# Kernel tuning notes

Measured on AMD Instinct MI355X. Metric: run time of the kernel, lower is better.

Reference implementation:

```python
import jax, jax.numpy as jnp
import numpy as np


def setup_inputs() -> dict:
    key = jax.random.key(0)
    k1, k2, k3 = jax.random.split(key, 3)
    vol_shape = (4, 1, 128, 192, 192)   # [B, C, D, H, W]
    dsc_shape = (4, 1, 8, 12, 12)       # PatchGAN-style discriminator logits
    return {
        "dsc_fake": jax.random.normal(k1, dsc_shape, dtype=jnp.float32),
        "predicts": jax.random.normal(k2, vol_shape, dtype=jnp.float32),
        "y_data": jax.random.normal(k3, vol_shape, dtype=jnp.float32),
        "zeros": jnp.zeros(dsc_shape, dtype=jnp.float32),
    }


def reference(dsc_fake, predicts, y_data, zeros):
    # BCE with logits (stable form), target = zeros
    bce = jnp.mean(
        jnp.maximum(dsc_fake, 0.0) - dsc_fake * zeros
        + jnp.log1p(jnp.exp(-jnp.abs(dsc_fake)))
    )
    # L1 loss between target volume and prediction
    g_loss_l1 = jnp.mean(jnp.abs(y_data - predicts))
    # Finite-difference gradient MSE along D, H, W (axes 2,3,4).
    # Original detaches to numpy, so this term carries no gradient.
    yd = jax.lax.stop_gradient(y_data)
    pr = jax.lax.stop_gradient(predicts)
    g_loss_gd = jnp.float32(0.0)
    for ax in (2, 3, 4):
        gy = jnp.abs(jnp.gradient(yd, axis=ax))   # central diff interior, one-sided edges
        gp = jnp.abs(jnp.gradient(pr, axis=ax))
        g_loss_gd = g_loss_gd + jnp.mean((gy - gp) ** 2)
    return bce + 100.0 * g_loss_l1 + 100.0 * g_loss_gd
```

## Files before the change

kernel.cpp:

```cpp
#include <hip/hip_runtime.h>
#include <math.h>

namespace {
constexpr int BATCH = 4;
constexpr int DDIM  = 128;
constexpr int HDIM  = 192;
constexpr int WDIM  = 192;
constexpr long long NTOT = (long long)BATCH * DDIM * HDIM * WDIM;
constexpr int GW   = WDIM / 4;
constexpr int HS4  = GW;
constexpr int DS4  = GW * HDIM;
constexpr int NDSC = 4 * 1 * 8 * 12 * 12;
constexpr int BLOCK = 256;
constexpr int DC    = 8;
constexpr int NCH   = DDIM / DC;
constexpr int NCOL  = BATCH * HDIM * GW;
constexpr int NTHREADS = NCOL * NCH;
constexpr int GRID  = NTHREADS / BLOCK;
}

__device__ __forceinline__ float4 ld4(const float* __restrict__ p, long long g) {
    return *(const float4*)(p + 4LL * g);
}

__global__ __launch_bounds__(BLOCK) void vol_kernel(const float* __restrict__ p,
                                                    const float* __restrict__ y,
                                                    float* __restrict__ part) {
    const int t    = blockIdx.x * BLOCK + threadIdx.x;
    const int lane = threadIdx.x & 63;
    const int gw   = t % GW;
    int rest       = t / GW;
    const int h    = rest % HDIM; rest /= HDIM;
    const int b    = rest % BATCH;
    const int d0   = (rest / BATCH) * DC;

    const int   hmo = (h > 0)        ? HS4 : 0;
    const int   hpo = (h < HDIM - 1) ? HS4 : 0;
    const float sh  = (h == 0 || h == HDIM - 1) ? 1.f : 0.5f;
    const float swx = (gw == 0)      ? 1.f : 0.5f;
    const float sww = (gw == GW - 1) ? 1.f : 0.5f;
    const bool needL = (lane == 0)  && (gw > 0);
    const bool needR = (lane == 63) && (gw < GW - 1);

    long long g = (((long long)b * DDIM + d0) * HDIM + h) * GW + gw;

    const long long gm = g - ((d0 > 0) ? DS4 : 0);
    float4 ym = ld4(y, gm), pm = ld4(p, gm);
    float4 yc = ld4(y, g),  pc = ld4(p, g);
    long long gn = g + DS4;
    float4 yn = ld4(y, gn), pn = ld4(p, gn);
    float4 yhm = ld4(y, g - hmo), yhp = ld4(y, g + hpo);
    float4 phm = ld4(p, g - hmo), php = ld4(p, g + hpo);
    float eLy = 0.f, eLp = 0.f, eRy = 0.f, eRp = 0.f;
    if (needL) { eLy = y[4LL * g - 1]; eLp = p[4LL * g - 1]; }
    if (needR) { eRy = y[4LL * g + 4]; eRp = p[4LL * g + 4]; }

    float l1 = 0.f, gd = 0.f;

    #pragma unroll
    for (int i = 0; i < DC; ++i) {
        const int d = d0 + i;

        float4 ynn, pnn, yhm2, yhp2, phm2, php2;
        float eLy2 = 0.f, eLp2 = 0.f, eRy2 = 0.f, eRp2 = 0.f;
        long long gnn = gn;
        if (i < DC - 1) {
            gnn = gn + ((d + 2 < DDIM) ? DS4 : 0);
            ynn  = ld4(y, gnn);      pnn  = ld4(p, gnn);
            yhm2 = ld4(y, gn - hmo); yhp2 = ld4(y, gn + hpo);
            phm2 = ld4(p, gn - hmo); php2 = ld4(p, gn + hpo);
            if (needL) { eLy2 = y[4LL * gn - 1]; eLp2 = p[4LL * gn - 1]; }
            if (needR) { eRy2 = y[4LL * gn + 4]; eRp2 = p[4LL * gn + 4]; }
        }

        const float sd = (d == 0 || d == DDIM - 1) ? 1.f : 0.5f;

        float Ly = __shfl_up(yc.w, 1, 64);
        float Lp = __shfl_up(pc.w, 1, 64);
        float Ry = __shfl_down(yc.x, 1, 64);
        float Rp = __shfl_down(pc.x, 1, 64);
        Ly = (lane == 0)  ? eLy : Ly;   Ly = gw ? Ly : yc.x;
        Lp = (lane == 0)  ? eLp : Lp;   Lp = gw ? Lp : pc.x;
        Ry = (lane == 63) ? eRy : Ry;   Ry = (gw == GW - 1) ? yc.w : Ry;
        Rp = (lane == 63) ? eRp : Rp;   Rp = (gw == GW - 1) ? pc.w : Rp;

        l1 += fabsf(yc.x - pc.x) + fabsf(yc.y - pc.y)
            + fabsf(yc.z - pc.z) + fabsf(yc.w - pc.w);

        float t0, gy, gp;
        gy = (yc.y - Ly) * swx;   gp = (pc.y - Lp) * swx;
        t0 = fabsf(gy) - fabsf(gp); gd += t0 * t0;
        gy = (yc.z - yc.x) * 0.5f; gp = (pc.z - pc.x) * 0.5f;
        t0 = fabsf(gy) - fabsf(gp); gd += t0 * t0;
        gy = (yc.w - yc.y) * 0.5f; gp = (pc.w - pc.y) * 0.5f;
        t0 = fabsf(gy) - fabsf(gp); gd += t0 * t0;
        gy = (Ry - yc.z) * sww;   gp = (Rp - pc.z) * sww;
        t0 = fabsf(gy) - fabsf(gp); gd += t0 * t0;

        t0 = fabsf((yhp.x - yhm.x) * sh) - fabsf((php.x - phm.x) * sh); gd += t0 * t0;
        t0 = fabsf((yhp.y - yhm.y) * sh) - fabsf((php.y - phm.y) * sh); gd += t0 * t0;
        t0 = fabsf((yhp.z - yhm.z) * sh) - fabsf((php.z - phm.z) * sh); gd += t0 * t0;
        t0 = fabsf((yhp.w - yhm.w) * sh) - fabsf((php.w - phm.w) * sh); gd += t0 * t0;

        t0 = fabsf((yn.x - ym.x) * sd) - fabsf((pn.x - pm.x) * sd); gd += t0 * t0;
        t0 = fabsf((yn.y - ym.y) * sd) - fabsf((pn.y - pm.y) * sd); gd += t0 * t0;
        t0 = fabsf((yn.z - ym.z) * sd) - fabsf((pn.z - pm.z) * sd); gd += t0 * t0;
        t0 = fabsf((yn.w - ym.w) * sd) - fabsf((pn.w - pm.w) * sd); gd += t0 * t0;

        if (i < DC - 1) {
            ym = yc; yc = yn; yn = ynn;
            pm = pc; pc = pn; pn = pnn;
            yhm = yhm2; yhp = yhp2; phm = phm2; php = php2;
            eLy = eLy2; eLp = eLp2; eRy = eRy2; eRp = eRp2;
            g = gn; gn = gnn;
        }
    }

    __shared__ float lds1[4], lds2[4];
    #pragma unroll
    for (int off = 32; off > 0; off >>= 1) {
        l1 += __shfl_down(l1, off, 64);
        gd += __shfl_down(gd, off, 64);
    }
    if ((threadIdx.x & 63) == 0) {
        lds1[threadIdx.x >> 6] = l1;
        lds2[threadIdx.x >> 6] = gd;
    }
    __syncthreads();
    if (threadIdx.x == 0) {
        part[2 * blockIdx.x]     = lds1[0] + lds1[1] + lds1[2] + lds1[3];
        part[2 * blockIdx.x + 1] = lds2[0] + lds2[1] + lds2[2] + lds2[3];
    }
}

__global__ __launch_bounds__(BLOCK) void finalize_kernel(const float* __restrict__ dsc,
                                                         const float* __restrict__ part,
                                                         float* __restrict__ out) {
    float l1 = 0.f, gd = 0.f, s = 0.f;
    for (int i = threadIdx.x; i < GRID; i += BLOCK) {
        l1 += part[2 * i];
        gd += part[2 * i + 1];
    }
    for (int i = threadIdx.x; i < NDSC; i += BLOCK) {
        const float x = dsc[i];
        s += fmaxf(x, 0.f) + log1pf(expf(-fabsf(x)));
    }
    __shared__ float a[4], c[4], e[4];
    #pragma unroll
    for (int off = 32; off > 0; off >>= 1) {
        l1 += __shfl_down(l1, off, 64);
        gd += __shfl_down(gd, off, 64);
        s  += __shfl_down(s,  off, 64);
    }
    if ((threadIdx.x & 63) == 0) {
        const int w = threadIdx.x >> 6;
        a[w] = l1; c[w] = gd; e[w] = s;
    }
    __syncthreads();
    if (threadIdx.x == 0) {
        const float bce = (e[0] + e[1] + e[2] + e[3]) / (float)NDSC;
        const float l1m = (a[0] + a[1] + a[2] + a[3]) / (float)NTOT;
        const float gdm = (c[0] + c[1] + c[2] + c[3]) / (float)NTOT;
        out[0] = bce + 100.f * (l1m + gdm);
    }
}

extern "C" void kernel_launch(void* const* d_in, const int* in_sizes, int n_in,
                              void* d_out, int out_size, void* d_ws, size_t ws_size,
                              hipStream_t stream) {
    const float* dsc_fake = (const float*)d_in[0];
    const float* predicts = (const float*)d_in[1];
    const float* y_data   = (const float*)d_in[2];
    float* part = (float*)d_ws;
    float* out  = (float*)d_out;

    vol_kernel<<<GRID, BLOCK, 0, stream>>>(predicts, y_data, part);
    finalize_kernel<<<1, BLOCK, 0, stream>>>(dsc_fake, part, out);
}
```

Measured before the change: 195.2 us.

## Stage H-tile planes in LDS with async global_load_lds triple buffering

Each block now owns an 8-row H tile (plus halo rows) across a 16-deep D chunk. It stages every D plane of y and p into LDS with global_load_lds, rotating three buffers so the plane two steps ahead loads while the current one is computed. H-neighbour, D-neighbour and W edge values are read from LDS instead of repeated global loads, which removes the redundant neighbour traffic of the per-thread streaming version. In exchange it adds a block barrier per D step, reloads halo rows, and runs 384-thread blocks with a large LDS footprint that may limit occupancy.

```diff
diff --git a/kernel.cpp b/kernel.cpp
--- a/kernel.cpp
+++ b/kernel.cpp
@@ -7,94 +7,127 @@
 constexpr int HDIM  = 192;
 constexpr int WDIM  = 192;
 constexpr long long NTOT = (long long)BATCH * DDIM * HDIM * WDIM;
-constexpr int GW   = WDIM / 4;
-constexpr int HS4  = GW;
-constexpr int DS4  = GW * HDIM;
-constexpr int NDSC = 4 * 1 * 8 * 12 * 12;
-constexpr int BLOCK = 256;
-constexpr int DC    = 8;
-constexpr int NCH   = DDIM / DC;
-constexpr int NCOL  = BATCH * HDIM * GW;
-constexpr int NTHREADS = NCOL * NCH;
-constexpr int GRID  = NTHREADS / BLOCK;
+constexpr int GW    = WDIM / 4;
+constexpr int NDSC  = 4 * 1 * 8 * 12 * 12;
+constexpr int TH    = 8;
+constexpr int SROWS = TH + 2;
+constexpr int SGRP  = SROWS * GW;
+constexpr int SFL   = SGRP * 4;
+constexpr int BLOCK = TH * GW;
+constexpr int NWAVE = BLOCK / 64;
+constexpr int NCHUNK = (SGRP + 63) / 64;
+constexpr int DC    = 16;
+constexpr int GRID  = BATCH * (HDIM / TH) * (DDIM / DC);
 }
 
 __device__ __forceinline__ float4 ld4(const float* __restrict__ p, long long g) {
     return *(const float4*)(p + 4LL * g);
+}
+
+__device__ __forceinline__ void stage(const float* __restrict__ vol, long long fbase,
+                                      float* lds, int wave, int lane) {
+    for (int c = wave; c < NCHUNK; c += NWAVE) {
+        const int gbase = (c == NCHUNK - 1) ? (SGRP - 64) : (c * 64);
+        const float* g = vol + fbase + 4LL * (gbase + lane);
+        __builtin_amdgcn_global_load_lds(
+            (const __attribute__((address_space(1))) void*)g,
+            (__attribute__((address_space(3))) void*)(lds + 4 * gbase),
+            16, 0, 0);
+    }
 }
 
 __global__ __launch_bounds__(BLOCK) void vol_kernel(const float* __restrict__ p,
                                                     const float* __restrict__ y,
                                                     float* __restrict__ part) {
-    const int t    = blockIdx.x * BLOCK + threadIdx.x;
-    const int lane = threadIdx.x & 63;
-    const int gw   = t % GW;
-    int rest       = t / GW;
-    const int h    = rest % HDIM; rest /= HDIM;
-    const int b    = rest % BATCH;
-    const int d0   = (rest / BATCH) * DC;
-
-    const int   hmo = (h > 0)        ? HS4 : 0;
-    const int   hpo = (h < HDIM - 1) ? HS4 : 0;
+    __shared__ __align__(16) float smem[3][2][SFL];
+
+    int bid = blockIdx.x;
+    const int dIdx = bid % (DDIM / DC); bid /= (DDIM / DC);
+    const int hIdx = bid % (HDIM / TH); bid /= (HDIM / TH);
+    const int b    = bid;
+    const int d0   = dIdx * DC;
+    const int h0   = hIdx * TH;
+
+    const int tid  = threadIdx.x;
+    const int lane = tid & 63;
+    const int wave = tid >> 6;
+    const int r    = tid / GW;
+    const int gw   = tid % GW;
+    const int h    = h0 + r;
+
+    const int g0     = (h0 == 0) ? 0 : ((h0 == HDIM - TH) ? (HDIM - SROWS) : (h0 - 1));
+    const int rowOff = h0 - g0;
+    const int sf     = ((r + rowOff) * GW + gw) * 4;
+
+    const int   hmF = ((h == 0)        ? 0 : -GW) * 4;
+    const int   hpF = ((h == HDIM - 1) ? 0 :  GW) * 4;
     const float sh  = (h == 0 || h == HDIM - 1) ? 1.f : 0.5f;
     const float swx = (gw == 0)      ? 1.f : 0.5f;
     const float sww = (gw == GW - 1) ? 1.f : 0.5f;
     const bool needL = (lane == 0)  && (gw > 0);
     const bool needR = (lane == 63) && (gw < GW - 1);
 
-    long long g = (((long long)b * DDIM + d0) * HDIM + h) * GW + gw;
-
-    const long long gm = g - ((d0 > 0) ? DS4 : 0);
-    float4 ym = ld4(y, gm), pm = ld4(p, gm);
-    float4 yc = ld4(y, g),  pc = ld4(p, g);
-    long long gn = g + DS4;
-    float4 yn = ld4(y, gn), pn = ld4(p, gn);
-    float4 yhm = ld4(y, g - hmo), yhp = ld4(y, g + hpo);
-    float4 phm = ld4(p, g - hmo), php = ld4(p, g + hpo);
-    float eLy = 0.f, eLp = 0.f, eRy = 0.f, eRp = 0.f;
-    if (needL) { eLy = y[4LL * g - 1]; eLp = p[4LL * g - 1]; }
-    if (needR) { eRy = y[4LL * g + 4]; eRp = p[4LL * g + 4]; }
+    const long long planeStride = (long long)HDIM * WDIM;
+    const long long volBase = (long long)b * DDIM * planeStride + (long long)g0 * WDIM;
+
+    float* curY = &smem[0][0][0]; float* curP = &smem[0][1][0];
+    float* nxtY = &smem[1][0][0]; float* nxtP = &smem[1][1][0];
+    float* freY = &smem[2][0][0]; float* freP = &smem[2][1][0];
+
+    stage(y, volBase + (long long)d0 * planeStride, curY, wave, lane);
+    stage(p, volBase + (long long)d0 * planeStride, curP, wave, lane);
+    stage(y, volBase + (long long)(d0 + 1) * planeStride, nxtY, wave, lane);
+    stage(p, volBase + (long long)(d0 + 1) * planeStride, nxtP, wave, lane);
+
+    const int dm = (d0 > 0) ? (d0 - 1) : 0;
+    const long long gown = (((long long)b * DDIM + dm) * HDIM + h) * GW + gw;
+    float4 ym = ld4(y, gown), pm = ld4(p, gown);
 
     float l1 = 0.f, gd = 0.f;
-
-    #pragma unroll
+    float4 yc, pc;
+
     for (int i = 0; i < DC; ++i) {
         const int d = d0 + i;
-
-        float4 ynn, pnn, yhm2, yhp2, phm2, php2;
-        float eLy2 = 0.f, eLp2 = 0.f, eRy2 = 0.f, eRp2 = 0.f;
-        long long gnn = gn;
-        if (i < DC - 1) {
-            gnn = gn + ((d + 2 < DDIM) ? DS4 : 0);
-            ynn  = ld4(y, gnn);      pnn  = ld4(p, gnn);
-            yhm2 = ld4(y, gn - hmo); yhp2 = ld4(y, gn + hpo);
-            phm2 = ld4(p, gn - hmo); php2 = ld4(p, gn + hpo);
-            if (needL) { eLy2 = y[4LL * gn - 1]; eLp2 = p[4LL * gn - 1]; }
-            if (needR) { eRy2 = y[4LL * gn + 4]; eRp2 = p[4LL * gn + 4]; }
+        __syncthreads();
+        if (i == 0) {
+            yc = *(const float4*)(curY + sf);
+            pc = *(const float4*)(curP + sf);
         }
-
-        const float sd = (d == 0 || d == DDIM - 1) ? 1.f : 0.5f;
+        if (i + 2 <= DC) {
+            const int dd = (d0 + i + 2 < DDIM) ? (d0 + i + 2) : (DDIM - 1);
+            stage(y, volBase + (long long)dd * planeStride, freY, wave, lane);
+            stage(p, volBase + (long long)dd * planeStride, freP, wave, lane);
+        }
+
+        const float4 yn  = *(const float4*)(nxtY + sf);
+        const float4 pn  = *(const float4*)(nxtP + sf);
+        const float4 yhm = *(const float4*)(curY + sf + hmF);
+        const float4 yhp = *(const float4*)(curY + sf + hpF);
+        const float4 phm = *(const float4*)(curP + sf + hmF);
+        const float4 php = *(const float4*)(curP + sf + hpF);
 
         float Ly = __shfl_up(yc.w, 1, 64);
         float Lp = __shfl_up(pc.w, 1, 64);
         float Ry = __shfl_down(yc.x, 1, 64);
         float Rp = __shfl_down(pc.x, 1, 64);
-        Ly = (lane == 0)  ? eLy : Ly;   Ly = gw ? Ly : yc.x;
-        Lp = (lane == 0)  ? eLp : Lp;   Lp = gw ? Lp : pc.x;
-        Ry = (lane == 63) ? eRy : Ry;   Ry = (gw == GW - 1) ? yc.w : Ry;
-        Rp = (lane == 63) ? eRp : Rp;   Rp = (gw == GW - 1) ? pc.w : Rp;
+        if (needL) { Ly = curY[sf - 1]; Lp = curP[sf - 1]; }
+        if (needR) { Ry = curY[sf + 4]; Rp = curP[sf + 4]; }
+        Ly = gw ? Ly : yc.x;             Lp = gw ? Lp : pc.x;
+        Ry = (gw == GW - 1) ? yc.w : Ry; Rp = (gw == GW - 1) ? pc.w : Rp;
+
+        const float sd = (d == 0 || d == DDIM - 1) ? 1.f : 0.5f;
 
         l1 += fabsf(yc.x - pc.x) + fabsf(yc.y - pc.y)
             + fabsf(yc.z - pc.z) + fabsf(yc.w - pc.w);
 
         float t0, gy, gp;
-        gy = (yc.y - Ly) * swx;   gp = (pc.y - Lp) * swx;
+        gy = (yc.y - Ly) * swx;    gp = (pc.y - Lp) * swx;
         t0 = fabsf(gy) - fabsf(gp); gd += t0 * t0;
         gy = (yc.z - yc.x) * 0.5f; gp = (pc.z - pc.x) * 0.5f;
         t0 = fabsf(gy) - fabsf(gp); gd += t0 * t0;
         gy = (yc.w - yc.y) * 0.5f; gp = (pc.w - pc.y) * 0.5f;
         t0 = fabsf(gy) - fabsf(gp); gd += t0 * t0;
-        gy = (Ry - yc.z) * sww;   gp = (Rp - pc.z) * sww;
+        gy = (Ry - yc.z) * sww;    gp = (Rp - pc.z) * sww;
         t0 = fabsf(gy) - fabsf(gp); gd += t0 * t0;
 
         t0 = fabsf((yhp.x - yhm.x) * sh) - fabsf((php.x - phm.x) * sh); gd += t0 * t0;
@@ -107,41 +140,37 @@
         t0 = fabsf((yn.z - ym.z) * sd) - fabsf((pn.z - pm.z) * sd); gd += t0 * t0;
         t0 = fabsf((yn.w - ym.w) * sd) - fabsf((pn.w - pm.w) * sd); gd += t0 * t0;
 
-        if (i < DC - 1) {
-            ym = yc; yc = yn; yn = ynn;
-            pm = pc; pc = pn; pn = pnn;
-            yhm = yhm2; yhp = yhp2; phm = phm2; php = php2;
-            eLy = eLy2; eLp = eLp2; eRy = eRy2; eRp = eRp2;
-            g = gn; gn = gnn;
-        }
-    }
-
-    __shared__ float lds1[4], lds2[4];
+        ym = yc; yc = yn; pm = pc; pc = pn;
+        float* tY = curY; curY = nxtY; nxtY = freY; freY = tY;
+        float* tP = curP; curP = nxtP; nxtP = freP; freP = tP;
+    }
+
+    __shared__ float red1[NWAVE], red2[NWAVE];
     #pragma unroll
     for (int off = 32; off > 0; off >>= 1) {
         l1 += __shfl_down(l1, off, 64);
         gd += __shfl_down(gd, off, 64);
     }
-    if ((threadIdx.x & 63) == 0) {
-        lds1[threadIdx.x >> 6] = l1;
-        lds2[threadIdx.x >> 6] = gd;
-    }
+    if (lane == 0) { red1[wave] = l1; red2[wave] = gd; }
     __syncthreads();
-    if (threadIdx.x == 0) {
-        part[2 * blockIdx.x]     = lds1[0] + lds1[1] + lds1[2] + lds1[3];
-        part[2 * blockIdx.x + 1] = lds2[0] + lds2[1] + lds2[2] + lds2[3];
-    }
-}
-
-__global__ __launch_bounds__(BLOCK) void finalize_kernel(const float* __restrict__ dsc,
-                                                         const float* __restrict__ part,
-                                                         float* __restrict__ out) {
+    if (tid == 0) {
+        float s1 = 0.f, s2 = 0.f;
+        #pragma unroll
+        for (int w = 0; w < NWAVE; ++w) { s1 += red1[w]; s2 += red2[w]; }
+        part[2 * blockIdx.x]     = s1;
+        part[2 * blockIdx.x + 1] = s2;
+    }
+}
+
+__global__ __launch_bounds__(256) void finalize_kernel(const float* __restrict__ dsc,
+                                                       const float* __restrict__ part,
+                                                       float* __restrict__ out) {
     float l1 = 0.f, gd = 0.f, s = 0.f;
-    for (int i = threadIdx.x; i < GRID; i += BLOCK) {
+    for (int i = threadIdx.x; i < GRID; i += 256) {
         l1 += part[2 * i];
         gd += part[2 * i + 1];
     }
-    for (int i = threadIdx.x; i < NDSC; i += BLOCK) {
+    for (int i = threadIdx.x; i < NDSC; i += 256) {
         const float x = dsc[i];
         s += fmaxf(x, 0.f) + log1pf(expf(-fabsf(x)));
     }
@@ -175,5 +204,5 @@
     float* out  = (float*)d_out;
 
     vol_kernel<<<GRID, BLOCK, 0, stream>>>(predicts, y_data, part);
-    finalize_kernel<<<1, BLOCK, 0, stream>>>(dsc_fake, part, out);
-}
+    finalize_kernel<<<1, 256, 0, stream>>>(dsc_fake, part, out);
+}
```

Result: no change. 197.1 us (+1.0%).
